# Performance work log

Hardware: AMD Instinct MI355X
Metric: run time of the kernel (lower is better)

The kernel has to match this reference:

```python
import jax, jax.numpy as jnp
import numpy as np

R = 4        # in_transformations == out_transformations
FS = 3       # filter_size
PAD = 1
STRIDE = 1


def setup_inputs() -> dict:
    key = jax.random.key(0)
    k1, k2, k3 = jax.random.split(key, 3)
    B, Cin, O, K = 16, 64, 64, 4
    Ctot = Cin * R  # 256
    x = jax.random.normal(k1, (B, Ctot, 64, 64), dtype=jnp.float32)
    # kernel bank: [num_dynamic_kernels, out_channels, in_channels, f, f]
    kernel_bank = jax.random.normal(k2, (K, O, Cin, FS, FS), dtype=jnp.float32) * 0.05
    # routing fc: Linear(total_in_channels -> num_kernels)
    fc_w = jax.random.normal(k3, (K, Ctot), dtype=jnp.float32) * 0.05
    fc_b = jnp.zeros((K,), dtype=jnp.float32)
    return {"x": x, "kernel_bank": kernel_bank, "fc_w": fc_w, "fc_b": fc_b}


def reference(x, kernel_bank, fc_w, fc_b):
    B, Ctot, H, W = x.shape
    K, O, Cin, f, _ = kernel_bank.shape
    # --- dynamic routing: global avg pool -> fc -> sigmoid ---
    pooled = x.mean(axis=(2, 3))                                  # [B, Ctot]
    coeffs = jax.nn.sigmoid(pooled @ fc_w.T + fc_b)               # [B, K]
    # --- per-sample kernel synthesis ---
    base = jnp.einsum('bk,kocij->bocij', coeffs, kernel_bank)     # [B, O, Cin, f, f]
    # rotations rot90^k for k in 0..R-1 (matches torch.rot90 dims=(-2,-1))
    rotated = jnp.stack([jnp.rot90(base, k, axes=(-2, -1)) for k in range(R)], axis=1)  # [B, R, O, Cin, f, f]
    # block kernel: block (r_out, r_in) uses rotation index (r_out - r_in) % R,
    # so the r_in sum of convs becomes one conv over all R*Cin input channels.
    r_out = jnp.arange(R)[:, None]
    r_in = jnp.arange(R)[None, :]
    idx = (r_out - r_in) % R                                      # [R, R]
    big = rotated[:, idx]                                         # [B, R_out, R_in, O, Cin, f, f]
    big = big.transpose(0, 1, 3, 2, 4, 5, 6).reshape(B, R * O, R * Cin, f, f)
    # --- per-sample conv (vmapped over batch; each sample has its own kernel) ---
    def conv_one(xi, wi):
        return jax.lax.conv_general_dilated(
            xi[None], wi,
            window_strides=(STRIDE, STRIDE),
            padding=[(PAD, PAD), (PAD, PAD)],
            dimension_numbers=('NCHW', 'OIHW', 'NCHW'))[0]
    return jax.vmap(conv_one)(x, big)                             # [B, R*O, H, W]
```

## Files before the change

### kernel.cpp

```cpp
#include <hip/hip_runtime.h>
#include <hip/hip_bf16.h>
#include <math.h>

#define BATCH 16
#define CT    256
#define HW    64
#define OCH   64
#define NK    4
#define HP    66
#define NPIX  4356

typedef __attribute__((ext_vector_type(4))) float  f32x4;
typedef __attribute__((ext_vector_type(8))) short  s16x8;
typedef __attribute__((ext_vector_type(4))) unsigned short u16x4;

#define GLOBAL_AS __attribute__((address_space(1)))
#define LDS_AS    __attribute__((address_space(3)))

__device__ __constant__ int c_rotsrc[4][9] = {
    {0,1,2,3,4,5,6,7,8},
    {2,5,8,1,4,7,0,3,6},
    {8,7,6,5,4,3,2,1,0},
    {6,3,0,7,4,1,8,5,2}
};

static __device__ inline unsigned short f2bf(float f) {
    union { __hip_bfloat16 h; unsigned short u; } cv;
    cv.h = __float2bfloat16(f);
    return cv.u;
}

__global__ __launch_bounds__(256) void xpose_pool(const float* __restrict__ x,
                                                  unsigned short* __restrict__ xTg,
                                                  float* __restrict__ partial) {
    const int ci0 = blockIdx.x * 64;
    const int g0  = ci0 >> 3;
    const int pr  = blockIdx.y;
    const int b   = blockIdx.z;
    const int t   = threadIdx.x;

    if (pr == 0 || pr == HP-1) {
        for (int u = t; u < 8*HP; u += 256) {
            int g = u / HP, c = u % HP;
            *(s16x8*)(xTg + ((((size_t)(b*32 + g0 + g))*NPIX) + pr*HP + c)*8) =
                (s16x8)(short)0;
        }
        return;
    }
    const int r = pr - 1;

    __shared__ unsigned short tile[64][70];
    const int cilH = t >> 4;
    const int c0   = (t & 15) * 4;
    #pragma unroll
    for (int i = 0; i < 4; ++i) {
        int cil = cilH + i*16;
        f32x4 v = *(const f32x4*)(x + (((size_t)(b*CT + ci0 + cil))*HW + r)*HW + c0);
        tile[cil][c0+0] = f2bf(v[0]);
        tile[cil][c0+1] = f2bf(v[1]);
        tile[cil][c0+2] = f2bf(v[2]);
        tile[cil][c0+3] = f2bf(v[3]);
        float s = v[0] + v[1] + v[2] + v[3];
        s += __shfl_xor(s, 1, 16);
        s += __shfl_xor(s, 2, 16);
        s += __shfl_xor(s, 4, 16);
        s += __shfl_xor(s, 8, 16);
        if ((t & 15) == 0)
            partial[((size_t)(b*HW) + r)*CT + ci0 + cil] = s;
    }
    __syncthreads();

    if (t < 16) {
        int g = t & 7, side = t >> 3;
        *(s16x8*)(xTg + ((((size_t)(b*32 + g0 + g))*NPIX) + pr*HP + side*(HP-1))*8) =
            (s16x8)(short)0;
    }
    #pragma unroll
    for (int i = 0; i < 4; ++i) {
        int u = i*256 + t;
        int c = u & 63, cil0 = (u >> 6) * 4;
        u16x4 w;
        w[0] = tile[cil0+0][c];
        w[1] = tile[cil0+1][c];
        w[2] = tile[cil0+2][c];
        w[3] = tile[cil0+3][c];
        *(u16x4*)(xTg + ((((size_t)(b*32 + g0 + (cil0>>3)))*NPIX) + pr*HP + c + 1)*8
                  + (cil0 & 4)) = w;
    }
}

__global__ __launch_bounds__(256) void coeff_kernel(const float* __restrict__ partial,
                                                    const float* __restrict__ fc_w,
                                                    const float* __restrict__ fc_b,
                                                    float* __restrict__ coeffs) {
    const int b = blockIdx.x;
    const int t = threadIdx.x;
    const float* pp = partial + (size_t)b*HW*CT + t;
    float s = 0.f;
    #pragma unroll 8
    for (int r = 0; r < HW; ++r) s += pp[(size_t)r*CT];
    __shared__ float pool[CT];
    pool[t] = s * (1.f / (HW*HW));
    __syncthreads();
    const int w = t >> 6, l = t & 63;
    float d = 0.f;
    for (int c = l; c < CT; c += 64) d += pool[c] * fc_w[w*CT + c];
    for (int off = 32; off; off >>= 1) d += __shfl_down(d, off, 64);
    if (l == 0)
        coeffs[b*NK + w] = 1.f / (1.f + expf(-(d + fc_b[w])));
}

__global__ __launch_bounds__(256) void bankrot_kernel(const float* __restrict__ bank,
                                                      float* __restrict__ P) {
    const int idx = blockIdx.x * 256 + threadIdx.x;
    const int o = idx & 63;
    const int c = (idx >> 6) & 63;
    const int k = idx >> 12;
    const float* bp = bank + ((size_t)((k*OCH + o)*64 + c))*9;
    float v[9];
    #pragma unroll
    for (int s = 0; s < 9; ++s) v[s] = bp[s];
    #pragma unroll
    for (int rr = 0; rr < 4; ++rr)
        #pragma unroll
        for (int s = 0; s < 9; ++s)
            P[(size_t)(((k*4 + rr)*9 + s))*4096 + c*64 + o] = v[c_rotsrc[rr][s]];
}

__global__ __launch_bounds__(256) void wbuild_kernel(const float* __restrict__ coeffs,
                                                     const float* __restrict__ P,
                                                     unsigned short* __restrict__ Wb) {
    const int cig = blockIdx.x;
    const int s   = blockIdx.y;
    const int co  = threadIdx.x;
    const int ro  = co >> 6;
    const int o   = co & 63;
    const int ri  = cig >> 3;
    const int rr  = (ro - ri) & 3;
    const int c8  = (cig & 7) * 8;

    float r[NK][8];
    #pragma unroll
    for (int k = 0; k < NK; ++k) {
        const float* pp = P + (size_t)(((k*4 + rr)*9 + s))*4096 + o;
        #pragma unroll
        for (int q = 0; q < 8; ++q)
            r[k][q] = pp[(c8 + q)*64];
    }
    #pragma unroll
    for (int b = 0; b < BATCH; ++b) {
        const float cf0 = coeffs[b*NK+0], cf1 = coeffs[b*NK+1];
        const float cf2 = coeffs[b*NK+2], cf3 = coeffs[b*NK+3];
        s16x8 w;
        #pragma unroll
        for (int q = 0; q < 8; ++q) {
            float v = cf0*r[0][q] + cf1*r[1][q] + cf2*r[2][q] + cf3*r[3][q];
            w[q] = (short)f2bf(v);
        }
        *(s16x8*)(Wb + ((((size_t)(b*9 + s)*32 + cig)*256 + co) << 3)) = w;
    }
}

#define SLAB_U  266
#define CHUNK_U 1064
#define BUF_U   1088
#define MF(A_, B_, C_) __builtin_amdgcn_mfma_f32_16x16x32_bf16(A_, B_, C_, 0, 0, 0)

__global__ __launch_bounds__(256, 2) void conv_mfma(
        const unsigned short* __restrict__ xTg,
        const unsigned short* __restrict__ Wb,
        float* __restrict__ out) {
    const int bid = blockIdx.x;
    const int b   = (bid & 7)*2 + ((bid >> 3) & 1);
    const int r0  = (bid >> 4) * 2;

    const int t    = threadIdx.x;
    const int w    = t >> 6;
    const int lane = t & 63;
    const int lo16 = lane & 15;
    const int hi4  = lane >> 4;

    __shared__ __align__(16) unsigned short Xs[2*BUF_U*8];

    f32x4 acc[4][8];
    #pragma unroll
    for (int f = 0; f < 4; ++f)
        #pragma unroll
        for (int p = 0; p < 8; ++p)
            acc[f][p] = (f32x4)0.f;

    const unsigned short* Wlane = Wb +
        (((size_t)(b*9*32) + hi4)*256 + w*64 + lo16)*8;

#define LOADA(DST, CH, S)                                                       \
    do {                                                                        \
        const unsigned short* wp = Wlane + (size_t)((S)*32 + (CH)*4)*2048;      \
        _Pragma("unroll")                                                       \
        for (int f_ = 0; f_ < 4; ++f_)                                          \
            DST[f_] = *(const s16x8*)(wp + f_*128);                             \
    } while (0)

#define STAGE(CH, BUF)                                                          \
    do {                                                                        \
        _Pragma("unroll")                                                       \
        for (int it = 0; it < 5; ++it) {                                        \
            int ubase = it*256 + w*64;                                          \
            if (ubase < CHUNK_U) {                                              \
                int u  = ubase + lane;                                          \
                int us = u > (CHUNK_U-3) ? (CHUNK_U-3) : u;  \
                int q  = us / SLAB_U;                                           \
                int pl = us - q*SLAB_U;                                         \
                const unsigned short* src = xTg +                               \
                    (((size_t)(b*32 + (CH)*4 + q))*NPIX + r0*HP + pl)*8;        \
                __builtin_amdgcn_global_load_lds(                               \
                    (const GLOBAL_AS void*)src,                                 \
                    (LDS_AS void*)(Xs + (size_t)((BUF)*BUF_U + ubase)*8),       \
                    16, 0, 0);                                                  \
            }                                                                   \
        }                                                                       \
    } while (0)

    STAGE(0, 0);
    __syncthreads();

    for (int ch = 0; ch < 8; ++ch) {
        s16x8 A[9][4];
        LOADA(A[0], ch, 0);
        LOADA(A[1], ch, 1);
        __builtin_amdgcn_sched_barrier(0);
        if (ch < 7) STAGE(ch+1, (ch+1) & 1);

        const char* Xb = (const char*)Xs + (ch & 1)*(BUF_U*16)
                         + hi4*(SLAB_U*16) + lo16*16;

        #pragma unroll
        for (int s = 0; s < 9; ++s) {
            if (s < 7) LOADA(A[s+2], ch, s+2);
            const int dr = s/3, dc = s%3;
            #pragma unroll
            for (int p = 0; p < 8; ++p) {
                const int pixbase = ((p>>2) + dr)*HP + dc + (p&3)*16;
                s16x8 bf = *(const s16x8*)(Xb + pixbase*16);
                acc[0][p] = MF(A[s][0], bf, acc[0][p]);
                acc[1][p] = MF(A[s][1], bf, acc[1][p]);
                acc[2][p] = MF(A[s][2], bf, acc[2][p]);
                acc[3][p] = MF(A[s][3], bf, acc[3][p]);
            }
        }
        __syncthreads();
    }
#undef STAGE
#undef LOADA

    #pragma unroll
    for (int f = 0; f < 4; ++f)
        #pragma unroll
        for (int p = 0; p < 8; ++p) {
            const int row = r0 + (p >> 2);
            const int colb = (p & 3)*16 + lo16;
            #pragma unroll
            for (int j = 0; j < 4; ++j) {
                int co = w*64 + f*16 + hi4*4 + j;
                out[(((size_t)(b*CT + co))*HW + row)*HW + colb] = acc[f][p][j];
            }
        }
}

extern "C" void kernel_launch(void* const* d_in, const int* in_sizes, int n_in,
                              void* d_out, int out_size, void* d_ws, size_t ws_size,
                              hipStream_t stream) {
    const float* x    = (const float*)d_in[0];
    const float* bank = (const float*)d_in[1];
    const float* fc_w = (const float*)d_in[2];
    const float* fc_b = (const float*)d_in[3];
    float* out = (float*)d_out;

    char* wsb = (char*)d_ws;
    float* partial = (float*)wsb;
    float* Prot    = (float*)wsb;
    float* coeffs  = (float*)(wsb + 2359296);
    unsigned short* Wb  = (unsigned short*)(wsb + 2360320);
    unsigned short* xTg = (unsigned short*)(wsb + 21234688);

    xpose_pool<<<dim3(4, HP, BATCH), 256, 0, stream>>>(x, xTg, partial);
    coeff_kernel<<<BATCH, 256, 0, stream>>>(partial, fc_w, fc_b, coeffs);
    bankrot_kernel<<<64, 256, 0, stream>>>(bank, Prot);
    wbuild_kernel<<<dim3(32, 9), 256, 0, stream>>>(coeffs, Prot, Wb);
    conv_mfma<<<512, 256, 0, stream>>>(xTg, Wb, out);
}
```

Measured before the change: 97.50 us.

## Split conv block output channels across two CTAs, shrink per-wave accumulators

Each conv block now covers 128 output channels instead of 256. The grid doubles to 1024 blocks, and the four waves are arranged as 2 channel-groups by 2 rows, so each wave holds 4x4 accumulators instead of 4x8. With launch bounds raised to 3 blocks per SIMD group, the aim is higher occupancy and more blocks to spread across CUs. The cost is that every input slab is now staged into LDS by two blocks, which doubles input traffic, and each wave does fewer MFMAs per weight fragment loaded.

```diff
diff --git a/kernel.cpp b/kernel.cpp
--- a/kernel.cpp
+++ b/kernel.cpp
@@ -10,9 +10,9 @@
 #define HP    66
 #define NPIX  4356
 
-typedef __attribute__((ext_vector_type(4))) float  f32x4;
-typedef __attribute__((ext_vector_type(8))) short  s16x8;
-typedef __attribute__((ext_vector_type(4))) unsigned short u16x4;
+typedef __attribute__((ext_vector_type(4)))  float  f32x4;
+typedef __attribute__((ext_vector_type(8)))  short  s16x8;
+typedef __attribute__((ext_vector_type(4)))  unsigned short u16x4;
 
 #define GLOBAL_AS __attribute__((address_space(1)))
 #define LDS_AS    __attribute__((address_space(3)))
@@ -166,31 +166,35 @@
 #define BUF_U   1088
 #define MF(A_, B_, C_) __builtin_amdgcn_mfma_f32_16x16x32_bf16(A_, B_, C_, 0, 0, 0)
 
-__global__ __launch_bounds__(256, 2) void conv_mfma(
+__global__ __launch_bounds__(256, 3) void conv_mfma(
         const unsigned short* __restrict__ xTg,
         const unsigned short* __restrict__ Wb,
         float* __restrict__ out) {
-    const int bid = blockIdx.x;
-    const int b   = (bid & 7)*2 + ((bid >> 3) & 1);
-    const int r0  = (bid >> 4) * 2;
+    const int bid  = blockIdx.x;
+    const int b    = (bid & 7)*2 + ((bid >> 3) & 1);
+    const int rest = bid >> 4;
+    const int coT  = rest & 1;
+    const int r0   = (rest >> 1) * 2;
 
     const int t    = threadIdx.x;
     const int w    = t >> 6;
     const int lane = t & 63;
     const int lo16 = lane & 15;
     const int hi4  = lane >> 4;
+    const int wco  = w & 1;
+    const int wrow = w >> 1;
 
     __shared__ __align__(16) unsigned short Xs[2*BUF_U*8];
 
-    f32x4 acc[4][8];
+    f32x4 acc[4][4];
     #pragma unroll
     for (int f = 0; f < 4; ++f)
         #pragma unroll
-        for (int p = 0; p < 8; ++p)
+        for (int p = 0; p < 4; ++p)
             acc[f][p] = (f32x4)0.f;
 
     const unsigned short* Wlane = Wb +
-        (((size_t)(b*9*32) + hi4)*256 + w*64 + lo16)*8;
+        (((size_t)(b*9*32) + hi4)*256 + coT*128 + wco*64 + lo16)*8;
 
 #define LOADA(DST, CH, S)                                                       \
     do {                                                                        \
@@ -237,30 +241,42 @@
         for (int s = 0; s < 9; ++s) {
             if (s < 7) LOADA(A[s+2], ch, s+2);
             const int dr = s/3, dc = s%3;
-            #pragma unroll
-            for (int p = 0; p < 8; ++p) {
-                const int pixbase = ((p>>2) + dr)*HP + dc + (p&3)*16;
-                s16x8 bf = *(const s16x8*)(Xb + pixbase*16);
-                acc[0][p] = MF(A[s][0], bf, acc[0][p]);
-                acc[1][p] = MF(A[s][1], bf, acc[1][p]);
-                acc[2][p] = MF(A[s][2], bf, acc[2][p]);
-                acc[3][p] = MF(A[s][3], bf, acc[3][p]);
-            }
+            const int rowoff = (wrow + dr)*HP + dc;
+            s16x8 bf0 = *(const s16x8*)(Xb + (rowoff +  0)*16);
+            s16x8 bf1 = *(const s16x8*)(Xb + (rowoff + 16)*16);
+            s16x8 bf2 = *(const s16x8*)(Xb + (rowoff + 32)*16);
+            s16x8 bf3 = *(const s16x8*)(Xb + (rowoff + 48)*16);
+            acc[0][0] = MF(A[s][0], bf0, acc[0][0]);
+            acc[1][0] = MF(A[s][1], bf0, acc[1][0]);
+            acc[2][0] = MF(A[s][2], bf0, acc[2][0]);
+            acc[3][0] = MF(A[s][3], bf0, acc[3][0]);
+            acc[0][1] = MF(A[s][0], bf1, acc[0][1]);
+            acc[1][1] = MF(A[s][1], bf1, acc[1][1]);
+            acc[2][1] = MF(A[s][2], bf1, acc[2][1]);
+            acc[3][1] = MF(A[s][3], bf1, acc[3][1]);
+            acc[0][2] = MF(A[s][0], bf2, acc[0][2]);
+            acc[1][2] = MF(A[s][1], bf2, acc[1][2]);
+            acc[2][2] = MF(A[s][2], bf2, acc[2][2]);
+            acc[3][2] = MF(A[s][3], bf2, acc[3][2]);
+            acc[0][3] = MF(A[s][0], bf3, acc[0][3]);
+            acc[1][3] = MF(A[s][1], bf3, acc[1][3]);
+            acc[2][3] = MF(A[s][2], bf3, acc[2][3]);
+            acc[3][3] = MF(A[s][3], bf3, acc[3][3]);
         }
         __syncthreads();
     }
 #undef STAGE
 #undef LOADA
 
+    const int row = r0 + wrow;
     #pragma unroll
     for (int f = 0; f < 4; ++f)
         #pragma unroll
-        for (int p = 0; p < 8; ++p) {
-            const int row = r0 + (p >> 2);
-            const int colb = (p & 3)*16 + lo16;
+        for (int p = 0; p < 4; ++p) {
+            const int colb = p*16 + lo16;
             #pragma unroll
             for (int j = 0; j < 4; ++j) {
-                int co = w*64 + f*16 + hi4*4 + j;
+                int co = coT*128 + wco*64 + f*16 + hi4*4 + j;
                 out[(((size_t)(b*CT + co))*HW + row)*HW + colb] = acc[f][p][j];
             }
         }
@@ -286,5 +302,5 @@
     coeff_kernel<<<BATCH, 256, 0, stream>>>(partial, fc_w, fc_b, coeffs);
     bankrot_kernel<<<64, 256, 0, stream>>>(bank, Prot);
     wbuild_kernel<<<dim3(32, 9), 256, 0, stream>>>(coeffs, Prot, Wb);
-    conv_mfma<<<512, 256, 0, stream>>>(xTg, Wb, out);
-}
+    conv_mfma<<<1024, 256, 0, stream>>>(xTg, Wb, out);
+}
```

After: 111.0 us. +13.9%, slower.
